# Optimization experiments

Hardware: AMD Instinct MI355X
Metric: run time of the kernel (lower is better)

The kernel has to match this reference:

```python
import jax, jax.numpy as jnp
import numpy as np
from jax import lax

TAU = 2.0      # LIF decay constant (source: tau = 2.0)
V_TH = 1.0     # spikingjelly LIFNode default threshold
ALPHA = 2.0    # ATan surrogate default alpha
BN_EPS = 1e-5


@jax.custom_vjp
def spike(v):
    # Heaviside with ATan surrogate gradient (spikingjelly surrogate.ATan)
    return (v >= V_TH).astype(v.dtype)

def _spike_fwd(v):
    return spike(v), v

def _spike_bwd(v, g):
    x = (jnp.pi / 2.0) * ALPHA * (v - V_TH)
    return (g * (ALPHA / 2.0) / (1.0 + x * x),)

spike.defvjp(_spike_fwd, _spike_bwd)


def lif_step(v, x):
    # leaky integrate: v += (x - (v - v_reset)) / tau, v_reset = 0
    v = v + (x - v) / TAU
    s = spike(v)
    # hard reset to 0; detach_reset=True -> stop_gradient on s in the reset path
    v = v * (1.0 - lax.stop_gradient(s))
    return v, s


def multistep_lif(x_seq):
    # x_seq: (T, ...) ; membrane state carried across T, initial v = 0
    v0 = jnp.zeros_like(x_seq[0])
    _, s_seq = lax.scan(lif_step, v0, x_seq)
    return s_seq


def setup_inputs() -> dict:
    key = jax.random.key(0)
    ks = jax.random.split(key, 3)
    bs, length, c_num, hidden = 64, 128, 32, 256
    x = jax.random.normal(ks[0], (bs, length, c_num), dtype=jnp.float32)
    conv_w = jax.random.normal(ks[1], (hidden, 1, 1, 3), dtype=jnp.float32) * 0.3
    conv_b = jnp.zeros((hidden,), jnp.float32)
    bn_gamma = jnp.ones((hidden,), jnp.float32)
    bn_beta = jnp.zeros((hidden,), jnp.float32)
    bn_mean = jnp.zeros((hidden,), jnp.float32)
    bn_var = jnp.ones((hidden,), jnp.float32)
    lin_w = jax.random.normal(ks[2], (hidden, hidden), dtype=jnp.float32) * (1.0 / np.sqrt(hidden))
    lin_b = jnp.zeros((hidden,), jnp.float32)
    return {"x": x, "conv_w": conv_w, "conv_b": conv_b, "bn_gamma": bn_gamma,
            "bn_beta": bn_beta, "bn_mean": bn_mean, "bn_var": bn_var,
            "lin_w": lin_w, "lin_b": lin_b}


def reference(x, conv_w, conv_b, bn_gamma, bn_beta, bn_mean, bn_var, lin_w, lin_b):
    bs, length, c_num = x.shape
    hidden = conv_w.shape[0]

    # ---- ConvEncoder ----
    xi = jnp.transpose(x, (0, 2, 1))[:, None]  # (bs, 1, c_num, length)
    enc = lax.conv_general_dilated(
        xi, conv_w, window_strides=(1, 1), padding=((0, 0), (1, 1)),
        dimension_numbers=("NCHW", "OIHW", "NCHW"))
    enc = enc + conv_b[None, :, None, None]
    # BatchNorm2d (eval mode, running stats)
    inv = bn_gamma * lax.rsqrt(bn_var + BN_EPS)
    enc = (enc - bn_mean[None, :, None, None]) * inv[None, :, None, None] + bn_beta[None, :, None, None]
    # multi-step LIF over channel dim T = hidden (as in source permute(1,0,2,3))
    enc = jnp.transpose(enc, (1, 0, 2, 3))          # (hidden, bs, c_num, length)
    spks_enc = multistep_lif(enc)                   # (hidden, bs, c_num, length)

    # ---- reshape to per-(bs*c_num) sequences of length `length` with feature hidden ----
    h = jnp.transpose(spks_enc, (1, 2, 3, 0)).reshape(bs * c_num, length, hidden)

    # ---- SpikeRNNCell recurrence over time (Linear + stateful LIF) ----
    def rnn_step(v, x_t):                           # x_t: (N, hidden)
        z = x_t @ lin_w.T + lin_b
        v = v + (z - v) / TAU
        s = spike(v)
        v = v * (1.0 - lax.stop_gradient(s))
        return v, s

    v0 = jnp.zeros((bs * c_num, hidden), x.dtype)
    _, s_seq = lax.scan(rnn_step, v0, jnp.transpose(h, (1, 0, 2)))  # (length, N, hidden)
    spks = s_seq[-1]                                # final-step spikes (N, hidden)

    spks = spks.reshape(bs, c_num * hidden, -1)     # (bs, c_num*hidden, 1)
    return jnp.transpose(spks, (0, 2, 1)), spks[:, :, -1]
```

## Files before the change

### kernel.cpp

```cpp
#include <hip/hip_runtime.h>
#include <stdint.h>

typedef unsigned short u16;
typedef unsigned int u32;
typedef unsigned long long u64;

typedef __attribute__((ext_vector_type(4))) int i32x4;

#define OFF_SBITS 0u
#define SBITS_BYTES (2048u * 128u * 32u)
#define OFF_WQ   (SBITS_BYTES)
#define WQ_BYTES (4u * 16384u)
#define OFF_SCL  (OFF_WQ + WQ_BYTES)

__global__ __launch_bounds__(256) void prep_enc_kernel(
    const float* __restrict__ x,
    const float* __restrict__ conv_w, const float* __restrict__ conv_b,
    const float* __restrict__ gamma,  const float* __restrict__ beta,
    const float* __restrict__ mean,   const float* __restrict__ var,
    const float* __restrict__ lin_w,  uint8_t* __restrict__ ws,
    u64* __restrict__ sbits) {
    int tid = threadIdx.x;
    int blk = blockIdx.x;
    if (blk < 256) {
        __shared__ float red[256];
        int j = blk, k = tid;
        float wv = lin_w[j * 256 + k];
        red[k] = fabsf(wv);
        __syncthreads();
        #pragma unroll
        for (int s = 128; s > 0; s >>= 1) {
            if (k < s) red[k] = fmaxf(red[k], red[k + s]);
            __syncthreads();
        }
        float m = red[0];
        float S = (m > 0.f) ? 127.0f / m : 0.f;
        int q = __float2int_rn(wv * S);
        int kstep = k >> 6, quad = (k >> 4) & 3, i = k & 15;
        ((int8_t*)(ws + OFF_WQ))[kstep * 16384 + (j * 4 + quad) * 16 + i] =
            (int8_t)q;
        if (k == 0) ((float*)(ws + OFF_SCL))[j] = m * (1.0f / 127.0f);
    } else {
        __shared__ float4 cfl[256];
        {
            int h = tid;
            float inv = gamma[h] / sqrtf(var[h] + 1e-5f);
            float K = (conv_b[h] - mean[h]) * inv + beta[h];
            cfl[h] = make_float4(conv_w[h * 3 + 0] * inv,
                                 conv_w[h * 3 + 1] * inv,
                                 conv_w[h * 3 + 2] * inv, K);
        }
        int p = (blk - 256) * 256 + tid;
        int c = p & 31;
        int l = (p >> 5) & 127;
        int b0 = p >> 12;
        int xb = b0 * 4096 + l * 32 + c;
        float xb0 = x[xb],            xb1 = x[xb + 131072];
        float xa0 = (l > 0)   ? x[xb - 32]          : 0.f;
        float xa1 = (l > 0)   ? x[xb + 131072 - 32] : 0.f;
        float xc0 = (l < 127) ? x[xb + 32]          : 0.f;
        float xc1 = (l < 127) ? x[xb + 131072 + 32] : 0.f;
        u64* d0 = sbits + ((size_t)(b0 * 32 + c) * 128 + (size_t)l) * 4;
        u64* d1 = d0 + (size_t)1024 * 512;

        __syncthreads();
        float v0 = 0.f, v1 = 0.f;
        u64 cur0 = 0ull, cur1 = 0ull;
        #pragma unroll 8
        for (int h = 0; h < 256; ++h) {
            float4 a = cfl[h];
            float e0 = fmaf(a.x, xa0, fmaf(a.y, xb0, fmaf(a.z, xc0, a.w)));
            float e1 = fmaf(a.x, xa1, fmaf(a.y, xb1, fmaf(a.z, xc1, a.w)));
            v0 = v0 + (e0 - v0) * 0.5f;
            v1 = v1 + (e1 - v1) * 0.5f;
            bool s0 = (v0 >= 1.0f);
            bool s1 = (v1 >= 1.0f);
            cur0 |= ((u64)(s0 ? 1u : 0u)) << (h & 63);
            cur1 |= ((u64)(s1 ? 1u : 0u)) << (h & 63);
            if ((h & 63) == 63) {
                d0[h >> 6] = cur0; d1[h >> 6] = cur1;
                cur0 = 0ull; cur1 = 0ull;
            }
            v0 = s0 ? 0.f : v0;
            v1 = s1 ? 0.f : v1;
        }
    }
}

#define AROW 12

__device__ __forceinline__ i32x4 expand_a16(u32 word, int hshift) {
    u32 h = (word >> hshift) & 0xFFFFu;
    i32x4 r;
    r[0] = (int)(((h         & 0xFu) * 0x204081u) & 0x01010101u);
    r[1] = (int)((((h >> 4)  & 0xFu) * 0x204081u) & 0x01010101u);
    r[2] = (int)((((h >> 8)  & 0xFu) * 0x204081u) & 0x01010101u);
    r[3] = (int)(((h >> 12)         * 0x204081u) & 0x01010101u);
    return r;
}

__global__ __launch_bounds__(256, 2) void gemm_scan_kernel(
    const u64* __restrict__ sbits,
    const uint4* __restrict__ wq,
    const float* __restrict__ lin_b,
    const float* __restrict__ sclp,
    float* __restrict__ out) {
    __shared__ __align__(16) uint8_t smem[34816];
    u32* Awords = (u32*)smem;

    int tid  = threadIdx.x;
    int n    = blockIdx.x;
    int lane = tid & 63;
    int w    = tid >> 6;
    int l15  = lane & 15;
    int quad = lane >> 4;
    int lb   = w * 256 + l15 * 4 + quad;
    int wsel = quad >> 1;
    int hsh  = (quad & 1) * 16;

    const i32x4* Wf = (const i32x4*)wq;

    float bias = lin_b[tid];
    float sc   = sclp[tid];

    i32x4 bb[2][4];
    #pragma unroll
    for (int nf = 0; nf < 4; ++nf)
        bb[0][nf] = Wf[(size_t)(nf * 64 + lb)];

    {
        const uint4* src = (const uint4*)(sbits + (size_t)n * 512);
        uint4 v = src[tid];
        *(uint4*)(Awords + (tid >> 1) * AROW + (tid & 1) * 4) = v;
    }

    i32x4 acc[8][4];
    #pragma unroll
    for (int mf = 0; mf < 8; ++mf)
        #pragma unroll
        for (int nf = 0; nf < 4; ++nf) {
            i32x4 z = {0, 0, 0, 0};
            acc[mf][nf] = z;
        }

    __syncthreads();

    u32 aw[8][4];
    #pragma unroll
    for (int mf = 0; mf < 8; ++mf)
        #pragma unroll
        for (int ks = 0; ks < 4; ++ks)
            aw[mf][ks] = Awords[(mf * 16 + l15) * AROW + ks * 2 + wsel];

    #pragma unroll
    for (int ks = 0; ks < 4; ++ks) {
        int c = ks & 1, nx = c ^ 1;
        if (ks < 3) {
            #pragma unroll
            for (int nf = 0; nf < 4; ++nf)
                bb[nx][nf] = Wf[(size_t)((ks + 1) * 1024 + nf * 64 + lb)];
        }
        i32x4 afr[8];
        #pragma unroll
        for (int mf = 0; mf < 8; ++mf)
            afr[mf] = expand_a16(aw[mf][ks], hsh);
        #pragma unroll
        for (int nf = 0; nf < 4; ++nf)
            #pragma unroll
            for (int mf = 0; mf < 8; ++mf)
                acc[mf][nf] = __builtin_amdgcn_mfma_i32_16x16x64_i8(
                    afr[mf], bb[c][nf], acc[mf][nf], 0, 0, 0);
    }

    __syncthreads();

    int* ZW = (int*)(smem + (size_t)w * 8704);
    float zsc = 0.5f * sc;
    float zbi = 0.5f * bias;
    float v = 0.f, sOut = 0.f;
    #pragma unroll
    for (int ph = 0; ph < 4; ++ph) {
        #pragma unroll
        for (int mm = 0; mm < 2; ++mm) {
            int mf = ph * 2 + mm;
            #pragma unroll
            for (int nf = 0; nf < 4; ++nf)
                #pragma unroll
                for (int r = 0; r < 4; ++r) {
                    int tl = mm * 16 + quad * 4 + r;
                    int jl = nf * 16 + l15;
                    ZW[tl * 68 + jl] = acc[mf][nf][r];
                }
        }
        float zh[32];
        #pragma unroll
        for (int tl = 0; tl < 32; ++tl)
            zh[tl] = fmaf((float)ZW[tl * 68 + lane], zsc, zbi);
        #pragma unroll
        for (int tl = 0; tl < 32; ++tl) {
            v = fmaf(0.5f, v, zh[tl]);
            bool s = (v >= 1.0f);
            if (ph == 3 && tl == 31) sOut = s ? 1.f : 0.f;
            v = s ? 0.f : v;
        }
    }
    out[(size_t)n * 256 + tid]           = sOut;
    out[524288u + (size_t)n * 256 + tid] = sOut;
}

extern "C" void kernel_launch(void* const* d_in, const int* in_sizes, int n_in,
                              void* d_out, int out_size, void* d_ws, size_t ws_size,
                              hipStream_t stream) {
    const float* x      = (const float*)d_in[0];
    const float* conv_w = (const float*)d_in[1];
    const float* conv_b = (const float*)d_in[2];
    const float* gamma  = (const float*)d_in[3];
    const float* beta   = (const float*)d_in[4];
    const float* mean   = (const float*)d_in[5];
    const float* var    = (const float*)d_in[6];
    const float* lin_w  = (const float*)d_in[7];
    const float* lin_b  = (const float*)d_in[8];
    uint8_t* ws = (uint8_t*)d_ws;
    float* out = (float*)d_out;

    hipLaunchKernelGGL(prep_enc_kernel, dim3(768), dim3(256), 0, stream,
                       x, conv_w, conv_b, gamma, beta, mean, var, lin_w,
                       ws, (u64*)(ws + OFF_SBITS));
    hipLaunchKernelGGL(gemm_scan_kernel, dim3(2048), dim3(256), 0, stream,
                       (const u64*)(ws + OFF_SBITS),
                       (const uint4*)(ws + OFF_WQ), lin_b,
                       (const float*)(ws + OFF_SCL), out);
}
```

Before: 121.6 us.

## Quantize linear weights to FP4 and use scaled f8f6f4 MFMA for GEMM

Replaces the int8 weight quantization with 4-bit FP4 (e2m1) codes packed two per byte, and turns the spike bits into FP4 values of 1.0 for the MI355X mfma_scale_f32_16x16x128_f8f6f4 instruction. This halves the K-step count and weight bytes, and the MFMA now accumulates in float. It also folds the 0.5 LIF factor into the encoder coefficients so the membrane update becomes a single fma. The price is much coarser weight quantization, which could flip spikes and break agreement with the float reference.

```diff
diff --git a/kernel.cpp b/kernel.cpp
--- a/kernel.cpp
+++ b/kernel.cpp
@@ -4,14 +4,17 @@
 typedef unsigned short u16;
 typedef unsigned int u32;
 typedef unsigned long long u64;
-
-typedef __attribute__((ext_vector_type(4))) int i32x4;
+typedef unsigned char u8;
+
+typedef __attribute__((ext_vector_type(4))) int   i32x4;
+typedef __attribute__((ext_vector_type(8))) int   i32x8;
+typedef __attribute__((ext_vector_type(4))) float f32x4;
 
 #define OFF_SBITS 0u
 #define SBITS_BYTES (2048u * 128u * 32u)
-#define OFF_WQ   (SBITS_BYTES)
-#define WQ_BYTES (4u * 16384u)
-#define OFF_SCL  (OFF_WQ + WQ_BYTES)
+#define OFF_WQ4  (SBITS_BYTES)
+#define WQ4_BYTES (2u * 32768u)
+#define OFF_SCL  (OFF_WQ4 + WQ4_BYTES)
 
 __global__ __launch_bounds__(256) void prep_enc_kernel(
     const float* __restrict__ x,
@@ -24,6 +27,7 @@
     int blk = blockIdx.x;
     if (blk < 256) {
         __shared__ float red[256];
+        __shared__ u8 nib[256];
         int j = blk, k = tid;
         float wv = lin_w[j * 256 + k];
         red[k] = fabsf(wv);
@@ -34,21 +38,35 @@
             __syncthreads();
         }
         float m = red[0];
-        float S = (m > 0.f) ? 127.0f / m : 0.f;
-        int q = __float2int_rn(wv * S);
-        int kstep = k >> 6, quad = (k >> 4) & 3, i = k & 15;
-        ((int8_t*)(ws + OFF_WQ))[kstep * 16384 + (j * 4 + quad) * 16 + i] =
-            (int8_t)q;
-        if (k == 0) ((float*)(ws + OFF_SCL))[j] = m * (1.0f / 127.0f);
+        float S = (m > 0.f) ? 6.0f / m : 0.f;
+        float v6 = wv * S;
+        float av = fabsf(v6);
+        int code;
+        if      (av < 0.25f) code = 0;
+        else if (av < 0.75f) code = 1;
+        else if (av < 1.25f) code = 2;
+        else if (av < 1.75f) code = 3;
+        else if (av < 2.5f)  code = 4;
+        else if (av < 3.5f)  code = 5;
+        else if (av < 5.0f)  code = 6;
+        else                 code = 7;
+        nib[k] = (u8)(((v6 < 0.f && code) ? 8 : 0) | code);
+        __syncthreads();
+        if (k < 128) {
+            u8 byte = (u8)(nib[2 * k] | (nib[2 * k + 1] << 4));
+            int ks = k >> 6, kb = (k >> 4) & 3, bi = k & 15;
+            (ws + OFF_WQ4)[ks * 32768 + (j * 4 + kb) * 16 + bi] = byte;
+        }
+        if (k == 0) ((float*)(ws + OFF_SCL))[j] = m * (1.0f / 12.0f);
     } else {
         __shared__ float4 cfl[256];
         {
             int h = tid;
             float inv = gamma[h] / sqrtf(var[h] + 1e-5f);
             float K = (conv_b[h] - mean[h]) * inv + beta[h];
-            cfl[h] = make_float4(conv_w[h * 3 + 0] * inv,
-                                 conv_w[h * 3 + 1] * inv,
-                                 conv_w[h * 3 + 2] * inv, K);
+            cfl[h] = make_float4(conv_w[h * 3 + 0] * inv * 0.5f,
+                                 conv_w[h * 3 + 1] * inv * 0.5f,
+                                 conv_w[h * 3 + 2] * inv * 0.5f, K * 0.5f);
         }
         int p = (blk - 256) * 256 + tid;
         int c = p & 31;
@@ -71,8 +89,8 @@
             float4 a = cfl[h];
             float e0 = fmaf(a.x, xa0, fmaf(a.y, xb0, fmaf(a.z, xc0, a.w)));
             float e1 = fmaf(a.x, xa1, fmaf(a.y, xb1, fmaf(a.z, xc1, a.w)));
-            v0 = v0 + (e0 - v0) * 0.5f;
-            v1 = v1 + (e1 - v1) * 0.5f;
+            v0 = fmaf(0.5f, v0, e0);
+            v1 = fmaf(0.5f, v1, e1);
             bool s0 = (v0 >= 1.0f);
             bool s1 = (v1 >= 1.0f);
             cur0 |= ((u64)(s0 ? 1u : 0u)) << (h & 63);
@@ -89,19 +107,16 @@
 
 #define AROW 12
 
-__device__ __forceinline__ i32x4 expand_a16(u32 word, int hshift) {
-    u32 h = (word >> hshift) & 0xFFFFu;
-    i32x4 r;
-    r[0] = (int)(((h         & 0xFu) * 0x204081u) & 0x01010101u);
-    r[1] = (int)((((h >> 4)  & 0xFu) * 0x204081u) & 0x01010101u);
-    r[2] = (int)((((h >> 8)  & 0xFu) * 0x204081u) & 0x01010101u);
-    r[3] = (int)(((h >> 12)         * 0x204081u) & 0x01010101u);
-    return r;
+__device__ __forceinline__ u32 spread_nib(u32 byte) {
+    u32 x = (byte | (byte << 12)) & 0x000F000Fu;
+    x = (x | (x << 6)) & 0x03030303u;
+    x = (x | (x << 3)) & 0x11111111u;
+    return x << 1;
 }
 
 __global__ __launch_bounds__(256, 2) void gemm_scan_kernel(
     const u64* __restrict__ sbits,
-    const uint4* __restrict__ wq,
+    const uint4* __restrict__ wq4,
     const float* __restrict__ lin_b,
     const float* __restrict__ sclp,
     float* __restrict__ out) {
@@ -115,10 +130,6 @@
     int l15  = lane & 15;
     int quad = lane >> 4;
     int lb   = w * 256 + l15 * 4 + quad;
-    int wsel = quad >> 1;
-    int hsh  = (quad & 1) * 16;
-
-    const i32x4* Wf = (const i32x4*)wq;
 
     float bias = lin_b[tid];
     float sc   = sclp[tid];
@@ -126,7 +137,7 @@
     i32x4 bb[2][4];
     #pragma unroll
     for (int nf = 0; nf < 4; ++nf)
-        bb[0][nf] = Wf[(size_t)(nf * 64 + lb)];
+        bb[0][nf] = ((const i32x4*)wq4)[(size_t)(nf * 64 + lb)];
 
     {
         const uint4* src = (const uint4*)(sbits + (size_t)n * 512);
@@ -134,48 +145,58 @@
         *(uint4*)(Awords + (tid >> 1) * AROW + (tid & 1) * 4) = v;
     }
 
-    i32x4 acc[8][4];
+    f32x4 acc[8][4];
     #pragma unroll
     for (int mf = 0; mf < 8; ++mf)
         #pragma unroll
         for (int nf = 0; nf < 4; ++nf) {
-            i32x4 z = {0, 0, 0, 0};
+            f32x4 z = {0.f, 0.f, 0.f, 0.f};
             acc[mf][nf] = z;
         }
 
     __syncthreads();
 
-    u32 aw[8][4];
+    u32 aw[8][2];
     #pragma unroll
     for (int mf = 0; mf < 8; ++mf)
         #pragma unroll
-        for (int ks = 0; ks < 4; ++ks)
-            aw[mf][ks] = Awords[(mf * 16 + l15) * AROW + ks * 2 + wsel];
-
-    #pragma unroll
-    for (int ks = 0; ks < 4; ++ks) {
+        for (int ks = 0; ks < 2; ++ks)
+            aw[mf][ks] = Awords[(mf * 16 + l15) * AROW + ks * 4 + quad];
+
+    #pragma unroll
+    for (int ks = 0; ks < 2; ++ks) {
         int c = ks & 1, nx = c ^ 1;
-        if (ks < 3) {
+        if (ks < 1) {
             #pragma unroll
             for (int nf = 0; nf < 4; ++nf)
-                bb[nx][nf] = Wf[(size_t)((ks + 1) * 1024 + nf * 64 + lb)];
-        }
-        i32x4 afr[8];
-        #pragma unroll
-        for (int mf = 0; mf < 8; ++mf)
-            afr[mf] = expand_a16(aw[mf][ks], hsh);
-        #pragma unroll
-        for (int nf = 0; nf < 4; ++nf)
+                bb[nx][nf] = ((const i32x4*)wq4)[(size_t)(2048 + nf * 64 + lb)];
+        }
+        #pragma unroll
+        for (int mf = 0; mf < 8; ++mf) {
+            u32 wbits = aw[mf][ks];
+            i32x8 afr;
+            afr[0] = (int)spread_nib(wbits & 0xFFu);
+            afr[1] = (int)spread_nib((wbits >> 8) & 0xFFu);
+            afr[2] = (int)spread_nib((wbits >> 16) & 0xFFu);
+            afr[3] = (int)spread_nib(wbits >> 24);
+            afr[4] = 0; afr[5] = 0; afr[6] = 0; afr[7] = 0;
             #pragma unroll
-            for (int mf = 0; mf < 8; ++mf)
-                acc[mf][nf] = __builtin_amdgcn_mfma_i32_16x16x64_i8(
-                    afr[mf], bb[c][nf], acc[mf][nf], 0, 0, 0);
+            for (int nf = 0; nf < 4; ++nf) {
+                i32x8 bfr;
+                bfr[0] = bb[c][nf][0]; bfr[1] = bb[c][nf][1];
+                bfr[2] = bb[c][nf][2]; bfr[3] = bb[c][nf][3];
+                bfr[4] = 0; bfr[5] = 0; bfr[6] = 0; bfr[7] = 0;
+                acc[mf][nf] = __builtin_amdgcn_mfma_scale_f32_16x16x128_f8f6f4(
+                    afr, bfr, acc[mf][nf], 4, 4,
+                    0, 0x7F7F7F7F, 0, 0x7F7F7F7F);
+            }
+        }
     }
 
     __syncthreads();
 
-    int* ZW = (int*)(smem + (size_t)w * 8704);
-    float zsc = 0.5f * sc;
+    float* ZW = (float*)(smem + (size_t)w * 8704);
+    float zsc = sc;
     float zbi = 0.5f * bias;
     float v = 0.f, sOut = 0.f;
     #pragma unroll
@@ -195,7 +216,7 @@
         float zh[32];
         #pragma unroll
         for (int tl = 0; tl < 32; ++tl)
-            zh[tl] = fmaf((float)ZW[tl * 68 + lane], zsc, zbi);
+            zh[tl] = fmaf(ZW[tl * 68 + lane], zsc, zbi);
         #pragma unroll
         for (int tl = 0; tl < 32; ++tl) {
             v = fmaf(0.5f, v, zh[tl]);
@@ -228,6 +249,6 @@
                        ws, (u64*)(ws + OFF_SBITS));
     hipLaunchKernelGGL(gemm_scan_kernel, dim3(2048), dim3(256), 0, stream,
                        (const u64*)(ws + OFF_SBITS),
-                       (const uint4*)(ws + OFF_WQ), lin_b,
+                       (const uint4*)(ws + OFF_WQ4), lin_b,
                        (const float*)(ws + OFF_SCL), out);
 }
```

After: 116.3 us. 1.05x faster.
